# Kernel tuning notes

Hardware: AMD Instinct MI355X
Metric: run time of the kernel (lower is better)

The kernel has to match this reference:

```python
import jax, jax.numpy as jnp
import numpy as np

N = 100000
E = 1000000
F_IN = 128
H = 64
C = 40


def _glorot(key, shape):
    fan_in, fan_out = shape[1], shape[0]
    lim = float(np.sqrt(6.0 / (fan_in + fan_out)))
    return jax.random.uniform(key, shape, jnp.float32, -lim, lim)


def setup_inputs() -> dict:
    key = jax.random.key(0)
    ks = jax.random.split(key, 8)
    x = jax.random.normal(ks[0], (N, F_IN), jnp.float32)
    edge_index = jax.random.randint(ks[1], (2, E), 0, N, jnp.int64)
    params = {
        # conv1: lin(F_IN->H), outer1(H->H), outer2(H->H)
        "w1_lin": _glorot(ks[2], (H, F_IN)), "b1_lin": jnp.zeros((H,), jnp.float32),
        "w1_o1": _glorot(ks[3], (H, H)), "b1_o1": jnp.zeros((H,), jnp.float32),
        "w1_o2": _glorot(ks[4], (H, H)), "b1_o2": jnp.zeros((H,), jnp.float32),
        # conv2: lin(H->C), outer1(C->C), outer2(C->C)
        "w2_lin": _glorot(ks[5], (C, H)), "b2_lin": jnp.zeros((C,), jnp.float32),
        "w2_o1": _glorot(ks[6], (C, C)), "b2_o1": jnp.zeros((C,), jnp.float32),
        "w2_o2": _glorot(ks[7], (C, C)), "b2_o2": jnp.zeros((C,), jnp.float32),
    }
    return {"x": x, "edge_index": edge_index, **params}


def gcn_conv(x, src, dst, w_lin, b_lin, w_o1, b_o1, w_o2, b_o2):
    # x: [N, Fin] -> lin -> [N, Fout]
    h = x @ w_lin.T + b_lin
    # propagate: gather h[src] ([E, Fout]) and scatter-add into dst;
    # self-loops (i -> i) are equivalent to adding h itself.
    agg = jax.ops.segment_sum(h[src], dst, num_segments=h.shape[0]) + h
    out = jax.nn.relu(agg)
    out = jax.nn.relu(out @ w_o1.T + b_o1)
    return out @ w_o2.T + b_o2


def reference(x, edge_index, w1_lin, b1_lin, w1_o1, b1_o1, w1_o2, b1_o2,
              w2_lin, b2_lin, w2_o1, b2_o1, w2_o2, b2_o2):
    src, dst = edge_index[0], edge_index[1]
    h = gcn_conv(x, src, dst, w1_lin, b1_lin, w1_o1, b1_o1, w1_o2, b1_o2)
    h = jax.nn.relu(h)
    # dropout is identity in eval mode (training=False)
    return gcn_conv(h, src, dst, w2_lin, b2_lin, w2_o1, b2_o1, w2_o2, b2_o2)
```

## Files before the change

kernel.cpp:

```cpp
#include <hip/hip_runtime.h>

static constexpr int FIN = 128;
static constexpr int HD  = 64;
static constexpr int CD  = 40;
static constexpr int S2  = 64;
static constexpr int SLB = 72;

typedef __attribute__((ext_vector_type(8))) short short8;
typedef __attribute__((ext_vector_type(4))) float f32x4;

__device__ __forceinline__ unsigned short f2b(float f)
{
    union { float f; unsigned u; } x; x.f = f;
    unsigned u = x.u;
    return (unsigned short)((u + 0x7FFF + ((u >> 16) & 1)) >> 16);
}
__device__ __forceinline__ float b2f(unsigned short b)
{
    union { unsigned u; float f; } x; x.u = ((unsigned)b) << 16;
    return x.f;
}

static constexpr int NBMAX = 512;
static constexpr int ACH   = 4096;

__global__ __launch_bounds__(256)
void prep_kernel(const float* __restrict__ w1_lin, const float* __restrict__ w1_o1,
                 const float* __restrict__ w1_o2, const float* __restrict__ w2_lin,
                 const float* __restrict__ w2_o1, const float* __restrict__ w2_o2,
                 unsigned short* __restrict__ wb, int* __restrict__ bucketCount)
{
    int i = blockIdx.x * 256 + threadIdx.x;
    if (i < NBMAX) bucketCount[i] = 0;
    if (i >= 25600) return;
    const float* src; int Kin, Kp, Oin, off;
    if (i < 8192)       { src = w1_lin; Kin = 128; Kp = 128; Oin = 64; off = 0; }
    else if (i < 12288) { src = w1_o1;  Kin = 64;  Kp = 64;  Oin = 64; off = 8192; }
    else if (i < 16384) { src = w1_o2;  Kin = 64;  Kp = 64;  Oin = 64; off = 12288; }
    else if (i < 19456) { src = w2_lin; Kin = 64;  Kp = 64;  Oin = 40; off = 16384; }
    else if (i < 22528) { src = w2_o1;  Kin = 40;  Kp = 64;  Oin = 40; off = 19456; }
    else                { src = w2_o2;  Kin = 40;  Kp = 64;  Oin = 40; off = 22528; }
    int j = i - off;
    int o = j / Kp, k = j - o * Kp;
    float v = (o < Oin && k < Kin) ? src[o * Kin + k] : 0.f;
    wb[i] = f2b(v);
}

template<int NKT, int NOT>
__device__ __forceinline__ void mfma_tile(const short8* a, const unsigned short* __restrict__ Wbf,
                                          int l16, int quad, f32x4* acc)
{
    constexpr int KP = NKT * 32;
#pragma unroll
    for (int ot = 0; ot < NOT; ++ot) {
        acc[ot] = (f32x4){0.f, 0.f, 0.f, 0.f};
        const unsigned short* Wrow = Wbf + (size_t)(ot * 16 + l16) * KP + quad * 8;
#pragma unroll
        for (int kt = 0; kt < NKT; ++kt) {
            short8 b = *reinterpret_cast<const short8*>(Wrow + kt * 32);
            acc[ot] = __builtin_amdgcn_mfma_f32_16x16x32_bf16(a[kt], b, acc[ot], 0, 0, 0);
        }
    }
}

__device__ __forceinline__ f32x4 mv16(const unsigned short* slab,
                                      const unsigned short* __restrict__ Wbf,
                                      int o, int l16, int quad)
{
    short8 a0 = *reinterpret_cast<const short8*>(&slab[l16 * SLB + quad * 8]);
    short8 a1 = *reinterpret_cast<const short8*>(&slab[l16 * SLB + 32 + quad * 8]);
    const unsigned short* Wrow = Wbf + (size_t)o * 64 + quad * 8;
    short8 b0 = *reinterpret_cast<const short8*>(Wrow);
    short8 b1 = *reinterpret_cast<const short8*>(Wrow + 32);
    f32x4 acc = (f32x4){0.f, 0.f, 0.f, 0.f};
    acc = __builtin_amdgcn_mfma_f32_16x16x32_bf16(a0, b0, acc, 0, 0, 0);
    acc = __builtin_amdgcn_mfma_f32_16x16x32_bf16(a1, b1, acc, 0, 0, 0);
    return acc;
}

__global__ __launch_bounds__(256)
void mv1_bhist_kernel(const float* __restrict__ x, const unsigned short* __restrict__ wb1_lin,
                      const float* __restrict__ b1_lin, unsigned short* __restrict__ h,
                      int n, int tgrid,
                      const int* __restrict__ dst, int* __restrict__ bucketCount, int e, int nb)
{
    __shared__ int cnt[NBMAX];
    if (blockIdx.x >= tgrid) {
        const int bb = blockIdx.x - tgrid;
        const int t = threadIdx.x;
        for (int j = t; j < nb; j += 256) cnt[j] = 0;
        __syncthreads();
        const int i0 = bb * ACH;
        const int i1 = min(e, i0 + ACH);
        for (int i = i0 + t; i < i1; i += 256)
            atomicAdd(&cnt[dst[i] >> 8], 1);
        __syncthreads();
        for (int j = t; j < nb; j += 256)
            if (cnt[j]) atomicAdd(&bucketCount[j], cnt[j]);
        return;
    }
    const int t = threadIdx.x, wave = t >> 6, lane = t & 63;
    const int quad = lane >> 4, l16 = lane & 15;
    const int n0 = blockIdx.x * 64, m0 = wave * 16;
    int row = n0 + m0 + l16; if (row >= n) row = n - 1;

    short8 a[4];
#pragma unroll
    for (int kt = 0; kt < 4; ++kt) {
        const float* p = x + (size_t)row * FIN + kt * 32 + quad * 8;
        float4 f0 = *reinterpret_cast<const float4*>(p);
        float4 f1 = *reinterpret_cast<const float4*>(p + 4);
        short8 v;
        v[0] = (short)f2b(f0.x); v[1] = (short)f2b(f0.y);
        v[2] = (short)f2b(f0.z); v[3] = (short)f2b(f0.w);
        v[4] = (short)f2b(f1.x); v[5] = (short)f2b(f1.y);
        v[6] = (short)f2b(f1.z); v[7] = (short)f2b(f1.w);
        a[kt] = v;
    }
    f32x4 acc[4];
    mfma_tile<4, 4>(a, wb1_lin, l16, quad, acc);
#pragma unroll
    for (int ot = 0; ot < 4; ++ot) {
        int o = ot * 16 + l16;
        float bv = b1_lin[o];
#pragma unroll
        for (int r = 0; r < 4; ++r) {
            int node = n0 + m0 + quad * 4 + r;
            if (node < n) h[(size_t)node * HD + o] = f2b(acc[ot][r] + bv);
        }
    }
}

__global__ __launch_bounds__(256)
void bscan_kernel(const int* __restrict__ bucketCount, int* __restrict__ bucketOff,
                  int* __restrict__ bucketCursor, int nb)
{
    __shared__ int sA[NBMAX], sB[NBMAX];
    const int t = threadIdx.x;
#pragma unroll
    for (int s = t; s < NBMAX; s += 256) sA[s] = (s < nb) ? bucketCount[s] : 0;
    __syncthreads();
    int* pa = sA; int* pb = sB;
    for (int off = 1; off < NBMAX; off <<= 1) {
#pragma unroll
        for (int s = t; s < NBMAX; s += 256)
            pb[s] = pa[s] + ((s >= off) ? pa[s - off] : 0);
        __syncthreads();
        int* tmp = pa; pa = pb; pb = tmp;
    }
#pragma unroll
    for (int s = t; s <= nb && s < NBMAX; s += 256) {
        int v = (s == 0) ? 0 : pa[s - 1];
        bucketOff[s] = v;
        if (s < nb) bucketCursor[s] = v;
    }
}

__global__ __launch_bounds__(256)
void bpart_kernel(const int* __restrict__ src, const int* __restrict__ dst,
                  int* __restrict__ bucketCursor, uint2* __restrict__ pairs,
                  int e, int nb)
{
    __shared__ int cnt[NBMAX];
    __shared__ int base[NBMAX];
    const int t = threadIdx.x;
    for (int j = t; j < nb; j += 256) cnt[j] = 0;
    __syncthreads();
    const int i0 = blockIdx.x * ACH;
    const int i1 = min(e, i0 + ACH);
    for (int i = i0 + t; i < i1; i += 256)
        atomicAdd(&cnt[dst[i] >> 8], 1);
    __syncthreads();
    for (int j = t; j < nb; j += 256) {
        int c = cnt[j];
        base[j] = c ? atomicAdd(&bucketCursor[j], c) : 0;
        cnt[j] = 0;
    }
    __syncthreads();
    for (int i = i0 + t; i < i1; i += 256) {
        int d = dst[i];
        int bkt = d >> 8;
        int pos = base[bkt] + atomicAdd(&cnt[bkt], 1);
        pairs[pos] = make_uint2((unsigned)d, (unsigned)src[i]);
    }
}

__global__ __launch_bounds__(256)
void bbuild_kernel(const uint2* __restrict__ pairs, const int* __restrict__ bucketOff,
                   int* __restrict__ rowptr_end, int* __restrict__ deg_g,
                   int* __restrict__ eidx, int n)
{
    __shared__ int deg[256], sA[256], sB[256], cur[256];
    const int t = threadIdx.x;
    const int b = blockIdx.x;
    const int node0 = b << 8;
    const int e0 = bucketOff[b], e1 = bucketOff[b + 1];

    deg[t] = 0;
    __syncthreads();
    for (int i = e0 + t; i < e1; i += 256)
        atomicAdd(&deg[pairs[i].x & 255], 1);
    __syncthreads();
    sA[t] = deg[t];
    __syncthreads();
    int* pa = sA; int* pb = sB;
    for (int off = 1; off < 256; off <<= 1) {
        pb[t] = pa[t] + ((t >= off) ? pa[t - off] : 0);
        __syncthreads();
        int* tmp = pa; pa = pb; pb = tmp;
    }
    const int node = node0 + t;
    if (node < n) {
        rowptr_end[node] = e0 + pa[t];
        deg_g[node] = deg[t];
    }
    cur[t] = pa[t] - deg[t];
    __syncthreads();
    for (int i = e0 + t; i < e1; i += 256) {
        uint2 p = pairs[i];
        int pos = e0 + atomicAdd(&cur[p.x & 255], 1);
        eidx[pos] = (int)p.y;
    }
}

template<int STRIDE, int LPN>
__device__ __forceinline__ void gather_relu_slab(
    const int* __restrict__ rowptr_end, const int* __restrict__ deg_g,
    const int* __restrict__ eidx, const unsigned short* __restrict__ h,
    unsigned short* slabA, int node0, int n, int wave, int grp, int l16)
{
    const int r16 = wave * 4 + grp;
    const int node = node0 + r16;
    const int nodec = (node < n) ? node : (n - 1);
    const bool act = (l16 < LPN);
    const int c0 = l16 * 4;
    const int g16 = grp * 16;

    float a0 = 0.f, a1 = 0.f, a2 = 0.f, a3 = 0.f;
    if (act) {
        ushort4 v = *reinterpret_cast<const ushort4*>(h + (size_t)nodec * STRIDE + c0);
        a0 = b2f(v.x); a1 = b2f(v.y); a2 = b2f(v.z); a3 = b2f(v.w);
    }
    int end   = rowptr_end[nodec];
    int start = end - deg_g[nodec];
    if (node >= n) end = start;

    for (int base = start; base < end; base += 16) {
        int m = min(16, end - base);
        int sv = (l16 < m) ? eidx[base + l16] : 0;
        int j = 0;
        for (; j + 4 <= m; j += 4) {
            int s0 = __shfl(sv, g16 + j,     64);
            int s1 = __shfl(sv, g16 + j + 1, 64);
            int s2 = __shfl(sv, g16 + j + 2, 64);
            int s3 = __shfl(sv, g16 + j + 3, 64);
            if (act) {
                ushort4 w0 = *reinterpret_cast<const ushort4*>(h + (size_t)s0 * STRIDE + c0);
                ushort4 w1 = *reinterpret_cast<const ushort4*>(h + (size_t)s1 * STRIDE + c0);
                ushort4 w2 = *reinterpret_cast<const ushort4*>(h + (size_t)s2 * STRIDE + c0);
                ushort4 w3 = *reinterpret_cast<const ushort4*>(h + (size_t)s3 * STRIDE + c0);
                a0 += b2f(w0.x); a1 += b2f(w0.y); a2 += b2f(w0.z); a3 += b2f(w0.w);
                a0 += b2f(w1.x); a1 += b2f(w1.y); a2 += b2f(w1.z); a3 += b2f(w1.w);
                a0 += b2f(w2.x); a1 += b2f(w2.y); a2 += b2f(w2.z); a3 += b2f(w2.w);
                a0 += b2f(w3.x); a1 += b2f(w3.y); a2 += b2f(w3.z); a3 += b2f(w3.w);
            }
        }
        for (; j < m; ++j) {
            int s = __shfl(sv, g16 + j, 64);
            if (act) {
                ushort4 v = *reinterpret_cast<const ushort4*>(h + (size_t)s * STRIDE + c0);
                a0 += b2f(v.x); a1 += b2f(v.y); a2 += b2f(v.z); a3 += b2f(v.w);
            }
        }
    }
    if (act) {
        ushort4 o;
        o.x = f2b(fmaxf(a0, 0.f)); o.y = f2b(fmaxf(a1, 0.f));
        o.z = f2b(fmaxf(a2, 0.f)); o.w = f2b(fmaxf(a3, 0.f));
        *reinterpret_cast<ushort4*>(&slabA[r16 * SLB + c0]) = o;
    }
}

__global__ __launch_bounds__(256)
void gchainB_kernel(const int* __restrict__ rowptr_end, const int* __restrict__ deg_g,
                    const int* __restrict__ eidx, const unsigned short* __restrict__ h,
                    const unsigned short* __restrict__ wo1, const float* __restrict__ bo1,
                    const unsigned short* __restrict__ wo2, const float* __restrict__ bo2,
                    const unsigned short* __restrict__ wlin, const float* __restrict__ blin,
                    unsigned short* __restrict__ out, int n, int ggrid,
                    const int4* __restrict__ csr_src, int4* __restrict__ csr_dst, int c4)
{
    if (blockIdx.x >= ggrid) {
        const int stride = (gridDim.x - ggrid) * 256;
        for (int i = (blockIdx.x - ggrid) * 256 + threadIdx.x; i < c4; i += stride)
            csr_dst[i] = csr_src[i];
        return;
    }

    __shared__ unsigned short slabA[16 * SLB];
    __shared__ unsigned short slabB[16 * SLB];
    const int t = threadIdx.x, wave = t >> 6, lane = t & 63;
    const int quad = lane >> 4, l16 = lane & 15;
    const int node0 = blockIdx.x * 16;

    gather_relu_slab<HD, 16>(rowptr_end, deg_g, eidx, h, slabA, node0, n, wave, quad, l16);
    __syncthreads();

    {
        int o = wave * 16 + l16;
        f32x4 acc = mv16(slabA, wo1, o, l16, quad);
        float bv = bo1[o];
#pragma unroll
        for (int r = 0; r < 4; ++r)
            slabB[(quad * 4 + r) * SLB + o] = f2b(fmaxf(acc[r] + bv, 0.f));
    }
    __syncthreads();
    {
        int o = wave * 16 + l16;
        f32x4 acc = mv16(slabB, wo2, o, l16, quad);
        float bv = bo2[o];
#pragma unroll
        for (int r = 0; r < 4; ++r)
            slabA[(quad * 4 + r) * SLB + o] = f2b(fmaxf(acc[r] + bv, 0.f));
    }
    __syncthreads();
    if (wave < 3) {
        int o = wave * 16 + l16;
        f32x4 acc = mv16(slabA, wlin, o, l16, quad);
        float bv = (o < CD) ? blin[o] : 0.f;
#pragma unroll
        for (int r = 0; r < 4; ++r) {
            int node = node0 + quad * 4 + r;
            if (node < n) {
                float v = (o < CD) ? (acc[r] + bv) : 0.f;
                out[(size_t)node * S2 + o] = f2b(v);
            }
        }
    }
    else {
        int o = 48 + l16;
#pragma unroll
        for (int r = 0; r < 4; ++r) {
            int node = node0 + quad * 4 + r;
            if (node < n) out[(size_t)node * S2 + o] = 0;
        }
    }
}

__global__ __launch_bounds__(256)
void gchainC_kernel(const int* __restrict__ rowptr_end, const int* __restrict__ deg_g,
                    const int* __restrict__ eidx, const unsigned short* __restrict__ h2,
                    const unsigned short* __restrict__ wo1, const float* __restrict__ bo1,
                    const unsigned short* __restrict__ wo2, const float* __restrict__ bo2,
                    float* __restrict__ out, int n)
{
    __shared__ unsigned short slabA[16 * SLB];
    __shared__ unsigned short slabB[16 * SLB];
    const int t = threadIdx.x, wave = t >> 6, lane = t & 63;
    const int quad = lane >> 4, l16 = lane & 15;
    const int node0 = blockIdx.x * 16;

    for (int i = t; i < 16 * 16; i += 256) {
        int rr = i >> 4, cc = i & 15;
        slabA[rr * SLB + 48 + cc] = 0;
        slabB[rr * SLB + 48 + cc] = 0;
    }

    gather_relu_slab<S2, 12>(rowptr_end, deg_g, eidx, h2, slabA, node0, n, wave, quad, l16);
    __syncthreads();

    if (wave < 3) {
        int o = wave * 16 + l16;
        f32x4 acc = mv16(slabA, wo1, o, l16, quad);
        float bv = (o < CD) ? bo1[o] : 0.f;
#pragma unroll
        for (int r = 0; r < 4; ++r) {
            float v = (o < CD) ? fmaxf(acc[r] + bv, 0.f) : 0.f;
            slabB[(quad * 4 + r) * SLB + o] = f2b(v);
        }
    }
    __syncthreads();
    if (wave < 3) {
        int o = wave * 16 + l16;
        f32x4 acc = mv16(slabB, wo2, o, l16, quad);
        if (o < CD) {
            float bv = bo2[o];
#pragma unroll
            for (int r = 0; r < 4; ++r) {
                int node = node0 + quad * 4 + r;
                if (node < n) out[(size_t)node * CD + o] = acc[r] + bv;
            }
        }
    }
}

extern "C" void kernel_launch(void* const* d_in, const int* in_sizes, int n_in,
                              void* d_out, int out_size, void* d_ws, size_t ws_size,
                              hipStream_t stream)
{
    const float* x      = (const float*)d_in[0];
    const int*   ei     = (const int*)d_in[1];
    const float* w1_lin = (const float*)d_in[2];
    const float* b1_lin = (const float*)d_in[3];
    const float* w1_o1  = (const float*)d_in[4];
    const float* b1_o1  = (const float*)d_in[5];
    const float* w1_o2  = (const float*)d_in[6];
    const float* b1_o2  = (const float*)d_in[7];
    const float* w2_lin = (const float*)d_in[8];
    const float* b2_lin = (const float*)d_in[9];
    const float* w2_o1  = (const float*)d_in[10];
    const float* b2_o1  = (const float*)d_in[11];
    const float* w2_o2  = (const float*)d_in[12];
    const float* b2_o2  = (const float*)d_in[13];

    const int n = in_sizes[0] / FIN;
    const int e = in_sizes[1] / 2;
    const int* src = ei;
    const int* dst = ei + e;

    unsigned short* ws0 = (unsigned short*)d_ws;
    unsigned short* ws2 = ws0 + (size_t)n * HD;
    unsigned short* wb  = ws2 + (size_t)n * S2;
    unsigned short* wb1_lin = wb;
    unsigned short* wb1_o1  = wb1_lin + 64 * 128;
    unsigned short* wb1_o2  = wb1_o1  + 64 * 64;
    unsigned short* wb2_lin = wb1_o2  + 64 * 64;
    unsigned short* wb2_o1  = wb2_lin + 48 * 64;
    unsigned short* wb2_o2  = wb2_o1  + 48 * 64;
    uint2* pairs        = (uint2*)(wb2_o2 + 48 * 64);
    int*   bucketCount  = (int*)(pairs + e);
    int*   bucketOff    = bucketCount + NBMAX;
    int*   bucketCursor = bucketOff + NBMAX + 1;
    float* outp = (float*)d_out;

    int* eidx   = (int*)d_out;
    int* deg    = eidx + e;
    int* rowptr = deg + n;
    int* ceidx   = (int*)pairs;
    int* cdeg    = ceidx + e;
    int* crowptr = cdeg + n;

    const int nb    = (n + 255) >> 8;
    const int agrid = (e + ACH - 1) / ACH;
    const int tgrid = (n + 63) / 64;
    const int ggrid = (n + 15) / 16;
    const int cgrid = 150;
    const int c4    = (e + 2 * n) / 4;

    prep_kernel<<<(25600 + 255) / 256, 256, 0, stream>>>(
        w1_lin, w1_o1, w1_o2, w2_lin, w2_o1, w2_o2, wb, bucketCount);

    mv1_bhist_kernel<<<tgrid + agrid, 256, 0, stream>>>(
        x, wb1_lin, b1_lin, ws0, n, tgrid, dst, bucketCount, e, nb);

    bscan_kernel<<<1, 256, 0, stream>>>(bucketCount, bucketOff, bucketCursor, nb);
    bpart_kernel<<<agrid, 256, 0, stream>>>(src, dst, bucketCursor, pairs, e, nb);
    bbuild_kernel<<<nb, 256, 0, stream>>>(pairs, bucketOff, rowptr, deg, eidx, n);

    gchainB_kernel<<<ggrid + cgrid, 256, 0, stream>>>(
        rowptr, deg, eidx, ws0, wb1_o1, b1_o1, wb1_o2, b1_o2, wb2_lin, b2_lin,
        ws2, n, ggrid, (const int4*)eidx, (int4*)ceidx, c4);

    gchainC_kernel<<<ggrid, 256, 0, stream>>>(
        crowptr, cdeg, ceidx, ws2, wb2_o1, b2_o1, wb2_o2, b2_o2, outp, n);
}
```

Measured before the change: 241.9 us.

## Split first-layer linear transform across edge partition and CSR build kernels

Moves the bucket histogram into the weight-prep kernel and splits the first linear transform (x @ W1) into two halves. One half runs alongside the bucket-partition kernel and the other alongside the CSR-build kernel. Bucket count zeroing becomes a memset. The aim is to fill idle CUs during the small, latency-bound graph-build kernels and shorten the serial chain. The fixed split point of 782 blocks assumes tgrid is larger than that, and it adds a memset launch.

```diff
diff --git a/kernel.cpp b/kernel.cpp
--- a/kernel.cpp
+++ b/kernel.cpp
@@ -24,14 +24,98 @@
 static constexpr int NBMAX = 512;
 static constexpr int ACH   = 4096;
 
-__global__ __launch_bounds__(256)
-void prep_kernel(const float* __restrict__ w1_lin, const float* __restrict__ w1_o1,
-                 const float* __restrict__ w1_o2, const float* __restrict__ w2_lin,
-                 const float* __restrict__ w2_o1, const float* __restrict__ w2_o2,
-                 unsigned short* __restrict__ wb, int* __restrict__ bucketCount)
-{
+template<int NKT, int NOT>
+__device__ __forceinline__ void mfma_tile(const short8* a, const unsigned short* __restrict__ Wbf,
+                                          int l16, int quad, f32x4* acc)
+{
+    constexpr int KP = NKT * 32;
+#pragma unroll
+    for (int ot = 0; ot < NOT; ++ot) {
+        acc[ot] = (f32x4){0.f, 0.f, 0.f, 0.f};
+        const unsigned short* Wrow = Wbf + (size_t)(ot * 16 + l16) * KP + quad * 8;
+#pragma unroll
+        for (int kt = 0; kt < NKT; ++kt) {
+            short8 b = *reinterpret_cast<const short8*>(Wrow + kt * 32);
+            acc[ot] = __builtin_amdgcn_mfma_f32_16x16x32_bf16(a[kt], b, acc[ot], 0, 0, 0);
+        }
+    }
+}
+
+__device__ __forceinline__ f32x4 mv16(const unsigned short* slab,
+                                      const unsigned short* __restrict__ Wbf,
+                                      int o, int l16, int quad)
+{
+    short8 a0 = *reinterpret_cast<const short8*>(&slab[l16 * SLB + quad * 8]);
+    short8 a1 = *reinterpret_cast<const short8*>(&slab[l16 * SLB + 32 + quad * 8]);
+    const unsigned short* Wrow = Wbf + (size_t)o * 64 + quad * 8;
+    short8 b0 = *reinterpret_cast<const short8*>(Wrow);
+    short8 b1 = *reinterpret_cast<const short8*>(Wrow + 32);
+    f32x4 acc = (f32x4){0.f, 0.f, 0.f, 0.f};
+    acc = __builtin_amdgcn_mfma_f32_16x16x32_bf16(a0, b0, acc, 0, 0, 0);
+    acc = __builtin_amdgcn_mfma_f32_16x16x32_bf16(a1, b1, acc, 0, 0, 0);
+    return acc;
+}
+
+__device__ __forceinline__ void mv1_body(const float* __restrict__ x,
+    const unsigned short* __restrict__ wb1_lin, const float* __restrict__ b1_lin,
+    unsigned short* __restrict__ h, int n, int vb)
+{
+    const int t = threadIdx.x, wave = t >> 6, lane = t & 63;
+    const int quad = lane >> 4, l16 = lane & 15;
+    const int n0 = vb * 64, m0 = wave * 16;
+    int row = n0 + m0 + l16; if (row >= n) row = n - 1;
+
+    short8 a[4];
+#pragma unroll
+    for (int kt = 0; kt < 4; ++kt) {
+        const float* p = x + (size_t)row * FIN + kt * 32 + quad * 8;
+        float4 f0 = *reinterpret_cast<const float4*>(p);
+        float4 f1 = *reinterpret_cast<const float4*>(p + 4);
+        short8 v;
+        v[0] = (short)f2b(f0.x); v[1] = (short)f2b(f0.y);
+        v[2] = (short)f2b(f0.z); v[3] = (short)f2b(f0.w);
+        v[4] = (short)f2b(f1.x); v[5] = (short)f2b(f1.y);
+        v[6] = (short)f2b(f1.z); v[7] = (short)f2b(f1.w);
+        a[kt] = v;
+    }
+    f32x4 acc[4];
+    mfma_tile<4, 4>(a, wb1_lin, l16, quad, acc);
+#pragma unroll
+    for (int ot = 0; ot < 4; ++ot) {
+        int o = ot * 16 + l16;
+        float bv = b1_lin[o];
+#pragma unroll
+        for (int r = 0; r < 4; ++r) {
+            int node = n0 + m0 + quad * 4 + r;
+            if (node < n) h[(size_t)node * HD + o] = f2b(acc[ot][r] + bv);
+        }
+    }
+}
+
+__global__ __launch_bounds__(256)
+void prep_bhist_kernel(const float* __restrict__ w1_lin, const float* __restrict__ w1_o1,
+                       const float* __restrict__ w1_o2, const float* __restrict__ w2_lin,
+                       const float* __restrict__ w2_o1, const float* __restrict__ w2_o2,
+                       unsigned short* __restrict__ wb, int wgrid,
+                       const int* __restrict__ dst, int* __restrict__ bucketCount,
+                       int e, int nb)
+{
+    __shared__ int cnt[NBMAX];
+    if (blockIdx.x >= wgrid) {
+        const int bb = blockIdx.x - wgrid;
+        const int t = threadIdx.x;
+        for (int j = t; j < nb; j += 256) cnt[j] = 0;
+        __syncthreads();
+        const int i0 = bb * ACH;
+        const int i1 = min(e, i0 + ACH);
+        for (int i = i0 + t; i < i1; i += 256)
+            atomicAdd(&cnt[dst[i] >> 8], 1);
+        __syncthreads();
+        for (int j = t; j < nb; j += 256)
+            if (cnt[j]) atomicAdd(&bucketCount[j], cnt[j]);
+        return;
+    }
     int i = blockIdx.x * 256 + threadIdx.x;
-    if (i < NBMAX) bucketCount[i] = 0;
     if (i >= 25600) return;
     const float* src; int Kin, Kp, Oin, off;
     if (i < 8192)       { src = w1_lin; Kin = 128; Kp = 128; Oin = 64; off = 0; }
@@ -46,91 +130,6 @@
     wb[i] = f2b(v);
 }
 
-template<int NKT, int NOT>
-__device__ __forceinline__ void mfma_tile(const short8* a, const unsigned short* __restrict__ Wbf,
-                                          int l16, int quad, f32x4* acc)
-{
-    constexpr int KP = NKT * 32;
-#pragma unroll
-    for (int ot = 0; ot < NOT; ++ot) {
-        acc[ot] = (f32x4){0.f, 0.f, 0.f, 0.f};
-        const unsigned short* Wrow = Wbf + (size_t)(ot * 16 + l16) * KP + quad * 8;
-#pragma unroll
-        for (int kt = 0; kt < NKT; ++kt) {
-            short8 b = *reinterpret_cast<const short8*>(Wrow + kt * 32);
-            acc[ot] = __builtin_amdgcn_mfma_f32_16x16x32_bf16(a[kt], b, acc[ot], 0, 0, 0);
-        }
-    }
-}
-
-__device__ __forceinline__ f32x4 mv16(const unsigned short* slab,
-                                      const unsigned short* __restrict__ Wbf,
-                                      int o, int l16, int quad)
-{
-    short8 a0 = *reinterpret_cast<const short8*>(&slab[l16 * SLB + quad * 8]);
-    short8 a1 = *reinterpret_cast<const short8*>(&slab[l16 * SLB + 32 + quad * 8]);
-    const unsigned short* Wrow = Wbf + (size_t)o * 64 + quad * 8;
-    short8 b0 = *reinterpret_cast<const short8*>(Wrow);
-    short8 b1 = *reinterpret_cast<const short8*>(Wrow + 32);
-    f32x4 acc = (f32x4){0.f, 0.f, 0.f, 0.f};
-    acc = __builtin_amdgcn_mfma_f32_16x16x32_bf16(a0, b0, acc, 0, 0, 0);
-    acc = __builtin_amdgcn_mfma_f32_16x16x32_bf16(a1, b1, acc, 0, 0, 0);
-    return acc;
-}
-
-__global__ __launch_bounds__(256)
-void mv1_bhist_kernel(const float* __restrict__ x, const unsigned short* __restrict__ wb1_lin,
-                      const float* __restrict__ b1_lin, unsigned short* __restrict__ h,
-                      int n, int tgrid,
-                      const int* __restrict__ dst, int* __restrict__ bucketCount, int e, int nb)
-{
-    __shared__ int cnt[NBMAX];
-    if (blockIdx.x >= tgrid) {
-        const int bb = blockIdx.x - tgrid;
-        const int t = threadIdx.x;
-        for (int j = t; j < nb; j += 256) cnt[j] = 0;
-        __syncthreads();
-        const int i0 = bb * ACH;
-        const int i1 = min(e, i0 + ACH);
-        for (int i = i0 + t; i < i1; i += 256)
-            atomicAdd(&cnt[dst[i] >> 8], 1);
-        __syncthreads();
-        for (int j = t; j < nb; j += 256)
-            if (cnt[j]) atomicAdd(&bucketCount[j], cnt[j]);
-        return;
-    }
-    const int t = threadIdx.x, wave = t >> 6, lane = t & 63;
-    const int quad = lane >> 4, l16 = lane & 15;
-    const int n0 = blockIdx.x * 64, m0 = wave * 16;
-    int row = n0 + m0 + l16; if (row >= n) row = n - 1;
-
-    short8 a[4];
-#pragma unroll
-    for (int kt = 0; kt < 4; ++kt) {
-        const float* p = x + (size_t)row * FIN + kt * 32 + quad * 8;
-        float4 f0 = *reinterpret_cast<const float4*>(p);
-        float4 f1 = *reinterpret_cast<const float4*>(p + 4);
-        short8 v;
-        v[0] = (short)f2b(f0.x); v[1] = (short)f2b(f0.y);
-        v[2] = (short)f2b(f0.z); v[3] = (short)f2b(f0.w);
-        v[4] = (short)f2b(f1.x); v[5] = (short)f2b(f1.y);
-        v[6] = (short)f2b(f1.z); v[7] = (short)f2b(f1.w);
-        a[kt] = v;
-    }
-    f32x4 acc[4];
-    mfma_tile<4, 4>(a, wb1_lin, l16, quad, acc);
-#pragma unroll
-    for (int ot = 0; ot < 4; ++ot) {
-        int o = ot * 16 + l16;
-        float bv = b1_lin[o];
-#pragma unroll
-        for (int r = 0; r < 4; ++r) {
-            int node = n0 + m0 + quad * 4 + r;
-            if (node < n) h[(size_t)node * HD + o] = f2b(acc[ot][r] + bv);
-        }
-    }
-}
-
 __global__ __launch_bounds__(256)
 void bscan_kernel(const int* __restrict__ bucketCount, int* __restrict__ bucketOff,
                   int* __restrict__ bucketCursor, int nb)
@@ -157,12 +156,18 @@
 }
 
 __global__ __launch_bounds__(256)
-void bpart_kernel(const int* __restrict__ src, const int* __restrict__ dst,
-                  int* __restrict__ bucketCursor, uint2* __restrict__ pairs,
-                  int e, int nb)
+void bpart_mv1_kernel(const int* __restrict__ src, const int* __restrict__ dst,
+                      int* __restrict__ bucketCursor, uint2* __restrict__ pairs,
+                      int e, int nb, int agrid,
+                      const float* __restrict__ x, const unsigned short* __restrict__ wb1_lin,
+                      const float* __restrict__ b1_lin, unsigned short* __restrict__ h, int n)
 {
     __shared__ int cnt[NBMAX];
     __shared__ int base[NBMAX];
+    if (blockIdx.x >= agrid) {
+        mv1_body(x, wb1_lin, b1_lin, h, n, blockIdx.x - agrid);
+        return;
+    }
     const int t = threadIdx.x;
     for (int j = t; j < nb; j += 256) cnt[j] = 0;
     __syncthreads();
@@ -186,11 +191,17 @@
 }
 
 __global__ __launch_bounds__(256)
-void bbuild_kernel(const uint2* __restrict__ pairs, const int* __restrict__ bucketOff,
-                   int* __restrict__ rowptr_end, int* __restrict__ deg_g,
-                   int* __restrict__ eidx, int n)
+void bbuild_mv1_kernel(const uint2* __restrict__ pairs, const int* __restrict__ bucketOff,
+                       int* __restrict__ rowptr_end, int* __restrict__ deg_g,
+                       int* __restrict__ eidx, int n, int nb, int mv1base,
+                       const float* __restrict__ x, const unsigned short* __restrict__ wb1_lin,
+                       const float* __restrict__ b1_lin, unsigned short* __restrict__ h)
 {
     __shared__ int deg[256], sA[256], sB[256], cur[256];
+    if (blockIdx.x >= nb) {
+        mv1_body(x, wb1_lin, b1_lin, h, n, mv1base + (int)blockIdx.x - nb);
+        return;
+    }
     const int t = threadIdx.x;
     const int b = blockIdx.x;
     const int node0 = b << 8;
@@ -446,16 +457,22 @@
     const int ggrid = (n + 15) / 16;
     const int cgrid = 150;
     const int c4    = (e + 2 * n) / 4;
-
-    prep_kernel<<<(25600 + 255) / 256, 256, 0, stream>>>(
-        w1_lin, w1_o1, w1_o2, w2_lin, w2_o1, w2_o2, wb, bucketCount);
-
-    mv1_bhist_kernel<<<tgrid + agrid, 256, 0, stream>>>(
-        x, wb1_lin, b1_lin, ws0, n, tgrid, dst, bucketCount, e, nb);
+    const int wgrid = (25600 + 255) / 256;
+    const int mv1a  = 782;
+    const int mv1b  = tgrid - mv1a;
+
+    hipMemsetAsync(bucketCount, 0, NBMAX * sizeof(int), stream);
+
+    prep_bhist_kernel<<<wgrid + agrid, 256, 0, stream>>>(
+        w1_lin, w1_o1, w1_o2, w2_lin, w2_o1, w2_o2, wb, wgrid, dst, bucketCount, e, nb);
 
     bscan_kernel<<<1, 256, 0, stream>>>(bucketCount, bucketOff, bucketCursor, nb);
-    bpart_kernel<<<agrid, 256, 0, stream>>>(src, dst, bucketCursor, pairs, e, nb);
-    bbuild_kernel<<<nb, 256, 0, stream>>>(pairs, bucketOff, rowptr, deg, eidx, n);
+
+    bpart_mv1_kernel<<<agrid + mv1a, 256, 0, stream>>>(
+        src, dst, bucketCursor, pairs, e, nb, agrid, x, wb1_lin, b1_lin, ws0, n);
+
+    bbuild_mv1_kernel<<<nb + mv1b, 256, 0, stream>>>(
+        pairs, bucketOff, rowptr, deg, eidx, n, nb, mv1a, x, wb1_lin, b1_lin, ws0);
 
     gchainB_kernel<<<ggrid + cgrid, 256, 0, stream>>>(
         rowptr, deg, eidx, ws0, wb1_o1, b1_o1, wb1_o2, b1_o2, wb2_lin, b2_lin,
```

Result: no change. 240.4 us (-0.6%).

## Fuse weight prep, first linear, histogram and scan into one kernel

Applied to the files above, without the earlier changes.

Merges the weight-conversion, first-layer projection with bucket histogram, and the bucket prefix-scan into a single launch. The last histogram block, found with an atomic done-counter, performs the scan. The first linear layer now reads fp32 weights directly and converts them to bf16 in registers, and a memset zeroes the counters. This removes two kernel launches and their serialization gaps, at the cost of redundant per-block weight conversion and a serial scan tail inside one block.

```diff
diff --git a/kernel.cpp b/kernel.cpp
--- a/kernel.cpp
+++ b/kernel.cpp
@@ -23,45 +23,6 @@
 
 static constexpr int NBMAX = 512;
 static constexpr int ACH   = 4096;
-
-__global__ __launch_bounds__(256)
-void prep_kernel(const float* __restrict__ w1_lin, const float* __restrict__ w1_o1,
-                 const float* __restrict__ w1_o2, const float* __restrict__ w2_lin,
-                 const float* __restrict__ w2_o1, const float* __restrict__ w2_o2,
-                 unsigned short* __restrict__ wb, int* __restrict__ bucketCount)
-{
-    int i = blockIdx.x * 256 + threadIdx.x;
-    if (i < NBMAX) bucketCount[i] = 0;
-    if (i >= 25600) return;
-    const float* src; int Kin, Kp, Oin, off;
-    if (i < 8192)       { src = w1_lin; Kin = 128; Kp = 128; Oin = 64; off = 0; }
-    else if (i < 12288) { src = w1_o1;  Kin = 64;  Kp = 64;  Oin = 64; off = 8192; }
-    else if (i < 16384) { src = w1_o2;  Kin = 64;  Kp = 64;  Oin = 64; off = 12288; }
-    else if (i < 19456) { src = w2_lin; Kin = 64;  Kp = 64;  Oin = 40; off = 16384; }
-    else if (i < 22528) { src = w2_o1;  Kin = 40;  Kp = 64;  Oin = 40; off = 19456; }
-    else                { src = w2_o2;  Kin = 40;  Kp = 64;  Oin = 40; off = 22528; }
-    int j = i - off;
-    int o = j / Kp, k = j - o * Kp;
-    float v = (o < Oin && k < Kin) ? src[o * Kin + k] : 0.f;
-    wb[i] = f2b(v);
-}
-
-template<int NKT, int NOT>
-__device__ __forceinline__ void mfma_tile(const short8* a, const unsigned short* __restrict__ Wbf,
-                                          int l16, int quad, f32x4* acc)
-{
-    constexpr int KP = NKT * 32;
-#pragma unroll
-    for (int ot = 0; ot < NOT; ++ot) {
-        acc[ot] = (f32x4){0.f, 0.f, 0.f, 0.f};
-        const unsigned short* Wrow = Wbf + (size_t)(ot * 16 + l16) * KP + quad * 8;
-#pragma unroll
-        for (int kt = 0; kt < NKT; ++kt) {
-            short8 b = *reinterpret_cast<const short8*>(Wrow + kt * 32);
-            acc[ot] = __builtin_amdgcn_mfma_f32_16x16x32_bf16(a[kt], b, acc[ot], 0, 0, 0);
-        }
-    }
-}
 
 __device__ __forceinline__ f32x4 mv16(const unsigned short* slab,
                                       const unsigned short* __restrict__ Wbf,
@@ -78,30 +39,13 @@
     return acc;
 }
 
-__global__ __launch_bounds__(256)
-void mv1_bhist_kernel(const float* __restrict__ x, const unsigned short* __restrict__ wb1_lin,
-                      const float* __restrict__ b1_lin, unsigned short* __restrict__ h,
-                      int n, int tgrid,
-                      const int* __restrict__ dst, int* __restrict__ bucketCount, int e, int nb)
-{
-    __shared__ int cnt[NBMAX];
-    if (blockIdx.x >= tgrid) {
-        const int bb = blockIdx.x - tgrid;
-        const int t = threadIdx.x;
-        for (int j = t; j < nb; j += 256) cnt[j] = 0;
-        __syncthreads();
-        const int i0 = bb * ACH;
-        const int i1 = min(e, i0 + ACH);
-        for (int i = i0 + t; i < i1; i += 256)
-            atomicAdd(&cnt[dst[i] >> 8], 1);
-        __syncthreads();
-        for (int j = t; j < nb; j += 256)
-            if (cnt[j]) atomicAdd(&bucketCount[j], cnt[j]);
-        return;
-    }
+__device__ __forceinline__ void mv1_body(const float* __restrict__ x,
+    const float* __restrict__ w1_lin, const float* __restrict__ b1_lin,
+    unsigned short* __restrict__ h, int n, int vb)
+{
     const int t = threadIdx.x, wave = t >> 6, lane = t & 63;
     const int quad = lane >> 4, l16 = lane & 15;
-    const int n0 = blockIdx.x * 64, m0 = wave * 16;
+    const int n0 = vb * 64, m0 = wave * 16;
     int row = n0 + m0 + l16; if (row >= n) row = n - 1;
 
     short8 a[4];
@@ -118,7 +62,23 @@
         a[kt] = v;
     }
     f32x4 acc[4];
-    mfma_tile<4, 4>(a, wb1_lin, l16, quad, acc);
+#pragma unroll
+    for (int ot = 0; ot < 4; ++ot) {
+        acc[ot] = (f32x4){0.f, 0.f, 0.f, 0.f};
+        const float* wp0 = w1_lin + (size_t)(ot * 16 + l16) * FIN + quad * 8;
+#pragma unroll
+        for (int kt = 0; kt < 4; ++kt) {
+            const float* wp = wp0 + kt * 32;
+            float4 g0 = *reinterpret_cast<const float4*>(wp);
+            float4 g1 = *reinterpret_cast<const float4*>(wp + 4);
+            short8 b;
+            b[0] = (short)f2b(g0.x); b[1] = (short)f2b(g0.y);
+            b[2] = (short)f2b(g0.z); b[3] = (short)f2b(g0.w);
+            b[4] = (short)f2b(g1.x); b[5] = (short)f2b(g1.y);
+            b[6] = (short)f2b(g1.z); b[7] = (short)f2b(g1.w);
+            acc[ot] = __builtin_amdgcn_mfma_f32_16x16x32_bf16(a[kt], b, acc[ot], 0, 0, 0);
+        }
+    }
 #pragma unroll
     for (int ot = 0; ot < 4; ++ot) {
         int o = ot * 16 + l16;
@@ -132,28 +92,73 @@
 }
 
 __global__ __launch_bounds__(256)
-void bscan_kernel(const int* __restrict__ bucketCount, int* __restrict__ bucketOff,
-                  int* __restrict__ bucketCursor, int nb)
-{
+void fused1_kernel(const float* __restrict__ x, const float* __restrict__ w1_lin,
+                   const float* __restrict__ b1_lin, unsigned short* __restrict__ h,
+                   int n, int tgrid,
+                   const int* __restrict__ dst, int* __restrict__ bucketCount,
+                   int* __restrict__ bucketOff, int* __restrict__ bucketCursor,
+                   int* __restrict__ doneCnt, int e, int nb, int agrid,
+                   const float* __restrict__ w1_o1, const float* __restrict__ w1_o2,
+                   const float* __restrict__ w2_lin, const float* __restrict__ w2_o1,
+                   const float* __restrict__ w2_o2, unsigned short* __restrict__ wb)
+{
+    __shared__ int cnt[NBMAX];
     __shared__ int sA[NBMAX], sB[NBMAX];
+    __shared__ int isLast;
     const int t = threadIdx.x;
-#pragma unroll
-    for (int s = t; s < NBMAX; s += 256) sA[s] = (s < nb) ? bucketCount[s] : 0;
-    __syncthreads();
-    int* pa = sA; int* pb = sB;
-    for (int off = 1; off < NBMAX; off <<= 1) {
-#pragma unroll
-        for (int s = t; s < NBMAX; s += 256)
-            pb[s] = pa[s] + ((s >= off) ? pa[s - off] : 0);
+
+    if (blockIdx.x < tgrid) {
+        mv1_body(x, w1_lin, b1_lin, h, n, blockIdx.x);
+        return;
+    }
+    if (blockIdx.x < tgrid + agrid) {
+        const int bb = blockIdx.x - tgrid;
+        for (int j = t; j < nb; j += 256) cnt[j] = 0;
         __syncthreads();
-        int* tmp = pa; pa = pb; pb = tmp;
-    }
-#pragma unroll
-    for (int s = t; s <= nb && s < NBMAX; s += 256) {
-        int v = (s == 0) ? 0 : pa[s - 1];
-        bucketOff[s] = v;
-        if (s < nb) bucketCursor[s] = v;
-    }
+        const int i0 = bb * ACH;
+        const int i1 = min(e, i0 + ACH);
+        for (int i = i0 + t; i < i1; i += 256)
+            atomicAdd(&cnt[dst[i] >> 8], 1);
+        __syncthreads();
+        for (int j = t; j < nb; j += 256)
+            if (cnt[j]) atomicAdd(&bucketCount[j], cnt[j]);
+        __syncthreads();
+        if (t == 0) {
+            __threadfence();
+            isLast = (atomicAdd(doneCnt, 1) == agrid - 1) ? 1 : 0;
+        }
+        __syncthreads();
+        if (isLast) {
+            for (int s = t; s < NBMAX; s += 256)
+                sA[s] = (s < nb) ? atomicAdd(&bucketCount[s], 0) : 0;
+            __syncthreads();
+            int* pa = sA; int* pb = sB;
+            for (int off = 1; off < NBMAX; off <<= 1) {
+                for (int s = t; s < NBMAX; s += 256)
+                    pb[s] = pa[s] + ((s >= off) ? pa[s - off] : 0);
+                __syncthreads();
+                int* tmp = pa; pa = pb; pb = tmp;
+            }
+            for (int s = t; s <= nb && s < NBMAX; s += 256) {
+                int v = (s == 0) ? 0 : pa[s - 1];
+                bucketOff[s] = v;
+                if (s < nb) bucketCursor[s] = v;
+            }
+        }
+        return;
+    }
+    int i = (blockIdx.x - tgrid - agrid) * 256 + t;
+    if (i >= 17408) return;
+    const float* src; int Kin, Kp, Oin, base, wbo;
+    if (i < 4096)       { src = w1_o1;  Kin = 64; Kp = 64; Oin = 64; base = 0;     wbo = 8192; }
+    else if (i < 8192)  { src = w1_o2;  Kin = 64; Kp = 64; Oin = 64; base = 4096;  wbo = 12288; }
+    else if (i < 11264) { src = w2_lin; Kin = 64; Kp = 64; Oin = 40; base = 8192;  wbo = 16384; }
+    else if (i < 14336) { src = w2_o1;  Kin = 40; Kp = 64; Oin = 40; base = 11264; wbo = 19456; }
+    else                { src = w2_o2;  Kin = 40; Kp = 64; Oin = 40; base = 14336; wbo = 22528; }
+    int j = i - base;
+    int o = j / Kp, k = j - o * Kp;
+    float v = (o < Oin && k < Kin) ? src[o * Kin + k] : 0.f;
+    wb[wbo + j] = f2b(v);
 }
 
 __global__ __launch_bounds__(256)
@@ -421,16 +426,16 @@
     unsigned short* ws0 = (unsigned short*)d_ws;
     unsigned short* ws2 = ws0 + (size_t)n * HD;
     unsigned short* wb  = ws2 + (size_t)n * S2;
-    unsigned short* wb1_lin = wb;
-    unsigned short* wb1_o1  = wb1_lin + 64 * 128;
-    unsigned short* wb1_o2  = wb1_o1  + 64 * 64;
-    unsigned short* wb2_lin = wb1_o2  + 64 * 64;
-    unsigned short* wb2_o1  = wb2_lin + 48 * 64;
-    unsigned short* wb2_o2  = wb2_o1  + 48 * 64;
-    uint2* pairs        = (uint2*)(wb2_o2 + 48 * 64);
+    unsigned short* wb1_o1  = wb + 8192;
+    unsigned short* wb1_o2  = wb + 12288;
+    unsigned short* wb2_lin = wb + 16384;
+    unsigned short* wb2_o1  = wb + 19456;
+    unsigned short* wb2_o2  = wb + 22528;
+    uint2* pairs        = (uint2*)(wb + 25600);
     int*   bucketCount  = (int*)(pairs + e);
     int*   bucketOff    = bucketCount + NBMAX;
     int*   bucketCursor = bucketOff + NBMAX + 1;
+    int*   doneCnt      = bucketCursor + NBMAX;
     float* outp = (float*)d_out;
 
     int* eidx   = (int*)d_out;
@@ -446,15 +451,17 @@
     const int ggrid = (n + 15) / 16;
     const int cgrid = 150;
     const int c4    = (e + 2 * n) / 4;
-
-    prep_kernel<<<(25600 + 255) / 256, 256, 0, stream>>>(
-        w1_lin, w1_o1, w1_o2, w2_lin, w2_o1, w2_o2, wb, bucketCount);
-
-    mv1_bhist_kernel<<<tgrid + agrid, 256, 0, stream>>>(
-        x, wb1_lin, b1_lin, ws0, n, tgrid, dst, bucketCount, e, nb);
-
-    bscan_kernel<<<1, 256, 0, stream>>>(bucketCount, bucketOff, bucketCursor, nb);
+    const int pgrid = (17408 + 255) / 256;
+
+    hipMemsetAsync(bucketCount, 0, (3 * NBMAX + 2) * sizeof(int), stream);
+
+    fused1_kernel<<<tgrid + agrid + pgrid, 256, 0, stream>>>(
+        x, w1_lin, b1_lin, ws0, n, tgrid,
+        dst, bucketCount, bucketOff, bucketCursor, doneCnt, e, nb, agrid,
+        w1_o1, w1_o2, w2_lin, w2_o1, w2_o2, wb);
+
     bpart_kernel<<<agrid, 256, 0, stream>>>(src, dst, bucketCursor, pairs, e, nb);
+
     bbuild_kernel<<<nb, 256, 0, stream>>>(pairs, bucketOff, rowptr, deg, eidx, n);
 
     gchainB_kernel<<<ggrid + cgrid, 256, 0, stream>>>(
```

After: 253.7 us. 1.05x slower.
